# Optimization experiments

Hardware: AMD Instinct MI355X
Metric: run time of the kernel (lower is better)

The kernel has to match this reference:

```python
import jax, jax.numpy as jnp
import numpy as np

B, N, M, H, NH = 128, 4096, 64, 512, 4
IN, OUT = 256, 256
NH2 = 2 * NH  # read/write heads interleaved: even idx = read, odd idx = write
EPS = 1e-8


def setup_inputs() -> dict:
    key = jax.random.key(0)
    ks = jax.random.split(key, 20)
    nrm = lambda k, shape, s=0.05: (jax.random.normal(k, shape, jnp.float32) * s)
    return {
        'in_data': jax.random.normal(ks[0], (B, IN), jnp.float32),
        'memory': jax.random.normal(ks[1], (B, N, M), jnp.float32) * 0.1,
        'h_prev': jax.random.normal(ks[2], (B, H), jnp.float32),
        'c_prev': jax.random.normal(ks[3], (B, H), jnp.float32),
        'prev_reads': jax.random.normal(ks[4], (NH, B, M), jnp.float32),
        'prev_weights': jax.random.uniform(ks[5], (NH2, B, N), jnp.float32),
        # controller LSTMCell (input = in_data ++ prev_reads)
        'W_ih': nrm(ks[6], (4 * H, IN + NH * M)),
        'b_ih': jnp.zeros((4 * H,), jnp.float32),
        'W_hh': nrm(ks[7], (4 * H, H)),
        'b_hh': jnp.zeros((4 * H,), jnp.float32),
        # output layer over [h ++ reads]
        'W_out': nrm(ks[8], (OUT, H + NH * M)),
        'b_out': jnp.zeros((OUT,), jnp.float32),
        # per-head addressing params, stacked over the 2*NH heads (fed with c-state)
        'Wk': nrm(ks[9], (NH2, M, H)), 'bk': jnp.zeros((NH2, M), jnp.float32),
        'Wbeta': nrm(ks[10], (NH2, H)), 'bbeta': jnp.zeros((NH2,), jnp.float32),
        'Wg': nrm(ks[11], (NH2, H)), 'bg': jnp.zeros((NH2,), jnp.float32),
        'Ws': nrm(ks[12], (NH2, 3, H)), 'bs': jnp.zeros((NH2, 3), jnp.float32),
        'Wgam': nrm(ks[13], (NH2, H)), 'bgam': jnp.zeros((NH2,), jnp.float32),
        'We': nrm(ks[14], (NH2, M, H)), 'be': jnp.zeros((NH2, M), jnp.float32),
        'Wa': nrm(ks[15], (NH2, M, H)), 'ba': jnp.zeros((NH2, M), jnp.float32),
    }


def reference(in_data, memory, h_prev, c_prev, prev_reads, prev_weights,
              W_ih, b_ih, W_hh, b_hh, W_out, b_out,
              Wk, bk, Wbeta, bbeta, Wg, bg, Ws, bs, Wgam, bgam, We, be, Wa, ba):
    bsz = in_data.shape[0]
    # controller LSTM step on [x ++ prev_reads]
    x = jnp.concatenate([in_data, jnp.swapaxes(prev_reads, 0, 1).reshape(bsz, -1)], axis=-1)
    gates = x @ W_ih.T + h_prev @ W_hh.T + b_ih + b_hh
    gi, gf, gg, go = jnp.split(gates, 4, axis=-1)
    c = jax.nn.sigmoid(gf) * c_prev + jax.nn.sigmoid(gi) * jnp.tanh(gg)
    h = jax.nn.sigmoid(go) * jnp.tanh(c)  # |h| < 1, so clamp(-20, 20) is identity

    mem = memory
    reads = []
    for i in range(NH2):  # fixed small loop; even = read head, odd = write head
        keyv = c @ Wk[i].T + bk[i]                                    # [B, M]
        beta = jax.nn.softplus(c @ Wbeta[i] + bbeta[i])[:, None]      # [B, 1]
        g = jax.nn.sigmoid(c @ Wg[i] + bg[i])[:, None]                # [B, 1]
        s = jax.nn.softmax(c @ Ws[i].T + bs[i], axis=-1)              # [B, 3]
        gamma = 1.0 + jax.nn.softplus(c @ Wgam[i] + bgam[i])[:, None]  # [B, 1]
        # content addressing: cosine similarity, sharpened softmax
        sim = jnp.einsum('bnm,bm->bn', mem, keyv)
        sim = sim / (jnp.linalg.norm(mem, axis=-1) * jnp.linalg.norm(keyv, axis=-1, keepdims=True) + EPS)
        wc = jax.nn.softmax(beta * sim, axis=-1)
        # interpolate, circular shift (-1, 0, +1), sharpen
        wg_ = g * wc + (1.0 - g) * prev_weights[i]
        wsft = (s[:, 0:1] * jnp.roll(wg_, -1, axis=1)
                + s[:, 1:2] * wg_
                + s[:, 2:3] * jnp.roll(wg_, 1, axis=1))
        wpow = wsft ** gamma
        w = wpow / (jnp.sum(wpow, axis=1, keepdims=True) + EPS)
        if i % 2 == 0:
            reads.append(jnp.einsum('bn,bnm->bm', w, mem))
        else:
            e = jax.nn.sigmoid(c @ We[i].T + be[i])                   # erase [B, M]
            a = jnp.tanh(c @ Wa[i].T + ba[i])                         # add   [B, M]
            mem = mem * (1.0 - w[:, :, None] * e[:, None, :]) + w[:, :, None] * a[:, None, :]

    out = jax.nn.sigmoid(jnp.concatenate([h] + reads, axis=-1) @ W_out.T + b_out)
    return out
```

## Files before the change

### kernel.cpp

```cpp
#include <hip/hip_runtime.h>
#include <math.h>

#define BSZ 128
#define NN_ 4096
#define MM_ 64
#define HH_ 512
#define EPSF 1e-8f

__device__ __forceinline__ float sigmoidf_(float x) { return 1.0f / (1.0f + expf(-x)); }
__device__ __forceinline__ float softplusf_(float x) { return fmaxf(x, 0.0f) + log1pf(expf(-fabsf(x))); }

__global__ void k_build_x(const float* __restrict__ in_data, const float* __restrict__ prev_reads,
                          float* __restrict__ x) {
    int idx = blockIdx.x * blockDim.x + threadIdx.x;
    if (idx >= BSZ * 512) return;
    int b = idx >> 9, j = idx & 511;
    float v;
    if (j < 256) v = in_data[b * 256 + j];
    else {
        int hi = (j - 256) >> 6, m = (j - 256) & 63;
        v = prev_reads[(hi * BSZ + b) * 64 + m];
    }
    x[idx] = v;
}

__global__ __launch_bounds__(256) void k_gemm_atk(const float* __restrict__ A,
                                                  const float* __restrict__ W,
                                                  float* __restrict__ C, int Ncols, int K) {
    __shared__ float Alds[64 * 129];
    __shared__ float Wlds[64 * 65];
    int t = threadIdx.x;
    int k0 = blockIdx.y * 64;
    int n0 = blockIdx.x * 64;
    for (int i = 0; i < 8; ++i) {
        int f = t + 256 * i;
        int row = f >> 4, kk = (f & 15) * 4;
        float4 v = *(const float4*)(A + (size_t)row * K + k0 + kk);
        Alds[(kk + 0) * 129 + row] = v.x;
        Alds[(kk + 1) * 129 + row] = v.y;
        Alds[(kk + 2) * 129 + row] = v.z;
        Alds[(kk + 3) * 129 + row] = v.w;
    }
    for (int i = 0; i < 4; ++i) {
        int f = t + 256 * i;
        int o = f >> 4, kk = (f & 15) * 4;
        float4 v = *(const float4*)(W + (size_t)(n0 + o) * K + k0 + kk);
        Wlds[(kk + 0) * 65 + o] = v.x;
        Wlds[(kk + 1) * 65 + o] = v.y;
        Wlds[(kk + 2) * 65 + o] = v.z;
        Wlds[(kk + 3) * 65 + o] = v.w;
    }
    __syncthreads();
    int ob = (t & 15) * 4;
    int bb = (t >> 4) * 8;
    float acc[4][8];
#pragma unroll
    for (int i = 0; i < 4; ++i)
#pragma unroll
        for (int j = 0; j < 8; ++j) acc[i][j] = 0.f;
    for (int kk = 0; kk < 64; ++kk) {
        const float* wp = &Wlds[kk * 65 + ob];
        const float* ap = &Alds[kk * 129 + bb];
        float w0 = wp[0], w1 = wp[1], w2 = wp[2], w3 = wp[3];
#pragma unroll
        for (int j = 0; j < 8; ++j) {
            float av = ap[j];
            acc[0][j] = fmaf(w0, av, acc[0][j]);
            acc[1][j] = fmaf(w1, av, acc[1][j]);
            acc[2][j] = fmaf(w2, av, acc[2][j]);
            acc[3][j] = fmaf(w3, av, acc[3][j]);
        }
    }
#pragma unroll
    for (int i = 0; i < 4; ++i)
#pragma unroll
        for (int j = 0; j < 8; ++j)
            atomicAdd(&C[(size_t)(bb + j) * Ncols + n0 + ob + i], acc[i][j]);
}

__global__ void k_lstm(const float* __restrict__ gates, const float* __restrict__ b_ih,
                       const float* __restrict__ b_hh, const float* __restrict__ c_prev,
                       float* __restrict__ cbuf, float* __restrict__ hbuf) {
    int idx = blockIdx.x * blockDim.x + threadIdx.x;
    if (idx >= BSZ * HH_) return;
    int b = idx >> 9, j = idx & 511;
    const float* gr = gates + (size_t)b * 2048;
    float gi = gr[j]        + b_ih[j]        + b_hh[j];
    float gf = gr[512 + j]  + b_ih[512 + j]  + b_hh[512 + j];
    float gg = gr[1024 + j] + b_ih[1024 + j] + b_hh[1024 + j];
    float go = gr[1536 + j] + b_ih[1536 + j] + b_hh[1536 + j];
    float cc = sigmoidf_(gf) * c_prev[idx] + sigmoidf_(gi) * tanhf(gg);
    float hh = sigmoidf_(go) * tanhf(cc);
    cbuf[idx] = cc;
    hbuf[idx] = hh;
}

__global__ void k_build_whead(const float* __restrict__ Wk, const float* __restrict__ bk,
                              const float* __restrict__ Wbeta, const float* __restrict__ bbeta,
                              const float* __restrict__ Wg, const float* __restrict__ bg,
                              const float* __restrict__ Ws, const float* __restrict__ bs,
                              const float* __restrict__ Wgam, const float* __restrict__ bgam,
                              const float* __restrict__ We, const float* __restrict__ be,
                              const float* __restrict__ Wa, const float* __restrict__ ba,
                              float* __restrict__ Whead, float* __restrict__ bhead) {
    int idx = blockIdx.x * blockDim.x + threadIdx.x;
    if (idx >= 1600 * 512) return;
    int r = idx >> 9, k = idx & 511;
    float v = 0.f, bv = 0.f;
    if (r < 1584) {
        int i = r / 198, q = r - i * 198;
        if (q < 64)       { v = Wk[((i << 6) + q) * 512 + k];        bv = bk[(i << 6) + q]; }
        else if (q == 64) { v = Wbeta[i * 512 + k];                  bv = bbeta[i]; }
        else if (q == 65) { v = Wg[i * 512 + k];                     bv = bg[i]; }
        else if (q <= 68) { v = Ws[(i * 3 + q - 66) * 512 + k];      bv = bs[i * 3 + q - 66]; }
        else if (q == 69) { v = Wgam[i * 512 + k];                   bv = bgam[i]; }
        else if (q < 134) { v = We[((i << 6) + q - 70) * 512 + k];   bv = be[(i << 6) + q - 70]; }
        else              { v = Wa[((i << 6) + q - 134) * 512 + k];  bv = ba[(i << 6) + q - 134]; }
    }
    Whead[idx] = v;
    if (k == 0) bhead[r] = bv;
}

__global__ __launch_bounds__(256) void k_headact(const float* __restrict__ Chead, const float* __restrict__ bhead,
                                                 float* __restrict__ keys, float* __restrict__ knorm,
                                                 float* __restrict__ betaA, float* __restrict__ gA,
                                                 float* __restrict__ gammaA, float* __restrict__ sA,
                                                 float* __restrict__ eA, float* __restrict__ aA) {
    __shared__ float sk[64];
    __shared__ float s3[3];
    int blk = blockIdx.x;
    int i = blk >> 7, b = blk & 127;
    int q = threadIdx.x;
    float val = 0.f;
    if (q < 198) val = Chead[(size_t)b * 1600 + i * 198 + q] + bhead[i * 198 + q];
    if (q < 64) { keys[(size_t)(i * BSZ + b) * 64 + q] = val; sk[q] = val * val; }
    if (q >= 66 && q <= 68) s3[q - 66] = val;
    __syncthreads();
    if (q == 0) {
        float s = 0.f;
        for (int m2 = 0; m2 < 64; ++m2) s += sk[m2];
        knorm[i * BSZ + b] = sqrtf(s);
    }
    if (q == 64) betaA[i * BSZ + b] = softplusf_(val);
    if (q == 65) gA[i * BSZ + b] = sigmoidf_(val);
    if (q == 69) gammaA[i * BSZ + b] = 1.f + softplusf_(val);
    if (q == 66) {
        float mx = fmaxf(s3[0], fmaxf(s3[1], s3[2]));
        float e0 = expf(s3[0] - mx), e1 = expf(s3[1] - mx), e2 = expf(s3[2] - mx);
        float inv = 1.f / (e0 + e1 + e2);
        sA[(i * BSZ + b) * 3 + 0] = e0 * inv;
        sA[(i * BSZ + b) * 3 + 1] = e1 * inv;
        sA[(i * BSZ + b) * 3 + 2] = e2 * inv;
    }
    if (q >= 70 && q < 134)  eA[(size_t)(i * BSZ + b) * 64 + (q - 70)] = sigmoidf_(val);
    if (q >= 134 && q < 198) aA[(size_t)(i * BSZ + b) * 64 + (q - 134)] = tanhf(val);
}

__global__ __launch_bounds__(256) void k_pass2(const float* __restrict__ mem,
                                               const float* __restrict__ wbuf,
                                               const float* __restrict__ eA, const float* __restrict__ aA,
                                               const float* __restrict__ keys, const float* __restrict__ knorm,
                                               float* __restrict__ sims, float* __restrict__ r_out,
                                               int napply, int nsims, int sh0, int sh1,
                                               int read_state, int read_head, int read_idx) {
    __shared__ __align__(16) float rbuf[16][64];
    int t = threadIdx.x;
    int lane = t & 15, grp = t >> 4;
    int base = blockIdx.x * 64;
    int b = base >> 12;
    int m4 = lane * 4;
    float4 e1 = *(const float4*)(eA + (size_t)(1 * BSZ + b) * 64 + m4);
    float4 a1 = *(const float4*)(aA + (size_t)(1 * BSZ + b) * 64 + m4);
    float4 e3 = *(const float4*)(eA + (size_t)(3 * BSZ + b) * 64 + m4);
    float4 a3 = *(const float4*)(aA + (size_t)(3 * BSZ + b) * 64 + m4);
    float4 e5 = *(const float4*)(eA + (size_t)(5 * BSZ + b) * 64 + m4);
    float4 a5 = *(const float4*)(aA + (size_t)(5 * BSZ + b) * 64 + m4);
    float4 k0v = make_float4(0.f, 0.f, 0.f, 0.f), k1v = k0v;
    float kn0v = 0.f, kn1v = 0.f;
    if (nsims > 0) { k0v = *(const float4*)(keys + (size_t)(sh0 * BSZ + b) * 64 + m4); kn0v = knorm[sh0 * BSZ + b]; }
    if (nsims > 1) { k1v = *(const float4*)(keys + (size_t)(sh1 * BSZ + b) * 64 + m4); kn1v = knorm[sh1 * BSZ + b]; }
    const float* w1p = wbuf + (size_t)1 * BSZ * NN_;
    const float* w3p = wbuf + (size_t)3 * BSZ * NN_;
    const float* w5p = wbuf + (size_t)5 * BSZ * NN_;
    const float* wrp = (read_head >= 0) ? (wbuf + (size_t)read_head * BSZ * NN_) : nullptr;
    float* sim0 = sims + (size_t)sh0 * BSZ * NN_;
    float* sim1 = sims + (size_t)sh1 * BSZ * NN_;

    float4 racc = make_float4(0.f, 0.f, 0.f, 0.f);
    for (int it = 0; it < 4; ++it) {
        int row = base + it * 16 + grp;
        float4 m = *(const float4*)(mem + (size_t)row * 64 + m4);
        float4 mr = m;
        if (napply >= 1) {
            float w = w1p[row];
            m.x = m.x * (1.f - w * e1.x) + w * a1.x;
            m.y = m.y * (1.f - w * e1.y) + w * a1.y;
            m.z = m.z * (1.f - w * e1.z) + w * a1.z;
            m.w = m.w * (1.f - w * e1.w) + w * a1.w;
            if (read_state == 1) mr = m;
        }
        if (napply >= 2) {
            float w = w3p[row];
            m.x = m.x * (1.f - w * e3.x) + w * a3.x;
            m.y = m.y * (1.f - w * e3.y) + w * a3.y;
            m.z = m.z * (1.f - w * e3.z) + w * a3.z;
            m.w = m.w * (1.f - w * e3.w) + w * a3.w;
            if (read_state == 2) mr = m;
        }
        if (napply >= 3) {
            float w = w5p[row];
            m.x = m.x * (1.f - w * e5.x) + w * a5.x;
            m.y = m.y * (1.f - w * e5.y) + w * a5.y;
            m.z = m.z * (1.f - w * e5.z) + w * a5.z;
            m.w = m.w * (1.f - w * e5.w) + w * a5.w;
            if (read_state == 3) mr = m;
        }
        if (read_head >= 0) {
            float wr = wrp[row];
            racc.x = fmaf(wr, mr.x, racc.x);
            racc.y = fmaf(wr, mr.y, racc.y);
            racc.z = fmaf(wr, mr.z, racc.z);
            racc.w = fmaf(wr, mr.w, racc.w);
        }
        if (nsims > 0) {
            float d0 = m.x * k0v.x + m.y * k0v.y + m.z * k0v.z + m.w * k0v.w;
            float nn = m.x * m.x + m.y * m.y + m.z * m.z + m.w * m.w;
            float d1 = 0.f;
            if (nsims > 1) d1 = m.x * k1v.x + m.y * k1v.y + m.z * k1v.z + m.w * k1v.w;
#pragma unroll
            for (int off = 8; off >= 1; off >>= 1) {
                d0 += __shfl_xor(d0, off, 16);
                nn += __shfl_xor(nn, off, 16);
                if (nsims > 1) d1 += __shfl_xor(d1, off, 16);
            }
            if (lane == 0) {
                float nm = sqrtf(nn);
                sim0[row] = d0 / (nm * kn0v + EPSF);
                if (nsims > 1) sim1[row] = d1 / (nm * kn1v + EPSF);
            }
        }
    }
    if (read_head >= 0) {
        *(float4*)(&rbuf[grp][m4]) = racc;
        __syncthreads();
        if (t < 64) {
            float s = 0.f;
#pragma unroll
            for (int g2 = 0; g2 < 16; ++g2) s += rbuf[g2][t];
            atomicAdd(&r_out[(size_t)(read_idx * BSZ + b) * 64 + t], s);
        }
    }
}

__global__ __launch_bounds__(256) void k_weights(const float* __restrict__ sims,
                                                 const float* __restrict__ prev_w,
                                                 const float* __restrict__ betaA, const float* __restrict__ gA,
                                                 const float* __restrict__ gammaA, const float* __restrict__ sA,
                                                 float* __restrict__ wout_base, int head0) {
    __shared__ float wg[NN_];
    __shared__ float red[256];
    int h = head0 + blockIdx.y, b = blockIdx.x;
    int hb = h * BSZ + b;
    float beta = betaA[hb], g = gA[hb], gamma = gammaA[hb];
    float s0 = sA[hb * 3 + 0], s1 = sA[hb * 3 + 1], s2 = sA[hb * 3 + 2];
    const float* sim = sims + (size_t)hb * NN_;
    const float* pw = prev_w + (size_t)hb * NN_;
    float* wout = wout_base + (size_t)hb * NN_;
    int t = threadIdx.x;
    float tv[16];
    float lmax = -3.4e38f;
#pragma unroll
    for (int j = 0; j < 16; ++j) {
        float x = beta * sim[t + 256 * j];
        tv[j] = x;
        lmax = fmaxf(lmax, x);
    }
    red[t] = lmax; __syncthreads();
    for (int s = 128; s > 0; s >>= 1) { if (t < s) red[t] = fmaxf(red[t], red[t + s]); __syncthreads(); }
    float Mx = red[0]; __syncthreads();
    float lsum = 0.f;
#pragma unroll
    for (int j = 0; j < 16; ++j) { float ex = expf(tv[j] - Mx); tv[j] = ex; lsum += ex; }
    red[t] = lsum; __syncthreads();
    for (int s = 128; s > 0; s >>= 1) { if (t < s) red[t] += red[t + s]; __syncthreads(); }
    float invS = 1.f / red[0]; __syncthreads();
#pragma unroll
    for (int j = 0; j < 16; ++j) {
        int n = t + 256 * j;
        wg[n] = g * tv[j] * invS + (1.f - g) * pw[n];
    }
    __syncthreads();
    float lsum2 = 0.f;
#pragma unroll
    for (int j = 0; j < 16; ++j) {
        int n = t + 256 * j;
        float wsft = s0 * wg[(n + 1) & (NN_ - 1)] + s1 * wg[n] + s2 * wg[(n - 1) & (NN_ - 1)];
        float wp = powf(wsft, gamma);
        tv[j] = wp;
        lsum2 += wp;
    }
    red[t] = lsum2; __syncthreads();
    for (int s = 128; s > 0; s >>= 1) { if (t < s) red[t] += red[t + s]; __syncthreads(); }
    float inv2 = 1.f / (red[0] + EPSF);
#pragma unroll
    for (int j = 0; j < 16; ++j) wout[t + 256 * j] = tv[j] * inv2;
}

__global__ void k_build_cat(const float* __restrict__ hbuf, const float* __restrict__ rbuf,
                            float* __restrict__ cat) {
    int idx = blockIdx.x * blockDim.x + threadIdx.x;
    if (idx >= BSZ * 768) return;
    int b = idx / 768, j = idx - b * 768;
    float v;
    if (j < 512) v = hbuf[b * 512 + j];
    else {
        int ri = (j - 512) >> 6, m = (j - 512) & 63;
        v = rbuf[(ri * BSZ + b) * 64 + m];
    }
    cat[idx] = v;
}

__global__ void k_out(const float* __restrict__ outacc, const float* __restrict__ b_out,
                      float* __restrict__ out) {
    int idx = blockIdx.x * blockDim.x + threadIdx.x;
    if (idx >= BSZ * 256) return;
    out[idx] = sigmoidf_(outacc[idx] + b_out[idx & 255]);
}

extern "C" void kernel_launch(void* const* d_in, const int* in_sizes, int n_in,
                              void* d_out, int out_size, void* d_ws, size_t ws_size,
                              hipStream_t stream) {
    const float* in_data      = (const float*)d_in[0];
    const float* memory       = (const float*)d_in[1];
    const float* h_prev       = (const float*)d_in[2];
    const float* c_prev       = (const float*)d_in[3];
    const float* prev_reads   = (const float*)d_in[4];
    const float* prev_weights = (const float*)d_in[5];
    const float* W_ih = (const float*)d_in[6];
    const float* b_ih = (const float*)d_in[7];
    const float* W_hh = (const float*)d_in[8];
    const float* b_hh = (const float*)d_in[9];
    const float* W_out = (const float*)d_in[10];
    const float* b_out = (const float*)d_in[11];
    const float* Wk   = (const float*)d_in[12];
    const float* bk   = (const float*)d_in[13];
    const float* Wbeta = (const float*)d_in[14];
    const float* bbeta = (const float*)d_in[15];
    const float* Wg   = (const float*)d_in[16];
    const float* bg   = (const float*)d_in[17];
    const float* Ws   = (const float*)d_in[18];
    const float* bs   = (const float*)d_in[19];
    const float* Wgam = (const float*)d_in[20];
    const float* bgam = (const float*)d_in[21];
    const float* We   = (const float*)d_in[22];
    const float* be   = (const float*)d_in[23];
    const float* Wa   = (const float*)d_in[24];
    const float* ba   = (const float*)d_in[25];

    float* ws = (float*)d_ws;
    size_t o_gates  = 0;
    size_t o_chead  = o_gates + 262144;
    size_t o_r      = o_chead + 204800;
    size_t o_outacc = o_r + 32768;
    size_t zero_floats = o_outacc + 32768;
    size_t o_x     = zero_floats;
    size_t o_c     = o_x + 65536;
    size_t o_h     = o_c + 65536;
    size_t o_whead = o_h + 65536;
    size_t o_bhead = o_whead + 819200;
    size_t o_keys  = o_bhead + 2048;
    size_t o_knorm = o_keys + 65536;
    size_t o_beta  = o_knorm + 1024;
    size_t o_g     = o_beta + 1024;
    size_t o_gamma = o_g + 1024;
    size_t o_s     = o_gamma + 1024;
    size_t o_e     = o_s + 3072;
    size_t o_a     = o_e + 65536;
    size_t o_sims  = o_a + 65536;
    size_t o_w     = o_sims + 4194304;
    size_t o_cat   = o_w + 4194304;

    float* gates  = ws + o_gates;
    float* Chead  = ws + o_chead;
    float* rbuf   = ws + o_r;
    float* outacc = ws + o_outacc;
    float* xbuf   = ws + o_x;
    float* cbuf   = ws + o_c;
    float* hbuf   = ws + o_h;
    float* Whead  = ws + o_whead;
    float* bhead  = ws + o_bhead;
    float* keys   = ws + o_keys;
    float* knorm  = ws + o_knorm;
    float* betaA  = ws + o_beta;
    float* gA     = ws + o_g;
    float* gammaA = ws + o_gamma;
    float* sA     = ws + o_s;
    float* eA     = ws + o_e;
    float* aA     = ws + o_a;
    float* sims   = ws + o_sims;
    float* wbuf   = ws + o_w;
    float* cat    = ws + o_cat;

    hipMemsetAsync(d_ws, 0, zero_floats * sizeof(float), stream);

    k_build_x<<<256, 256, 0, stream>>>(in_data, prev_reads, xbuf);
    k_gemm_atk<<<dim3(32, 8), 256, 0, stream>>>(xbuf, W_ih, gates, 2048, 512);
    k_gemm_atk<<<dim3(32, 8), 256, 0, stream>>>(h_prev, W_hh, gates, 2048, 512);
    k_lstm<<<256, 256, 0, stream>>>(gates, b_ih, b_hh, c_prev, cbuf, hbuf);

    k_build_whead<<<3200, 256, 0, stream>>>(Wk, bk, Wbeta, bbeta, Wg, bg, Ws, bs,
                                            Wgam, bgam, We, be, Wa, ba, Whead, bhead);
    k_gemm_atk<<<dim3(25, 8), 256, 0, stream>>>(cbuf, Whead, Chead, 1600, 512);
    k_headact<<<1024, 256, 0, stream>>>(Chead, bhead, keys, knorm, betaA, gA, gammaA, sA, eA, aA);

    const int PB = BSZ * NN_ / 64;
    k_pass2<<<PB, 256, 0, stream>>>(memory, wbuf, eA, aA, keys, knorm, sims, rbuf,
                                    0, 2, 0, 1, -1, -1, 0);
    k_weights<<<dim3(128, 2), 256, 0, stream>>>(sims, prev_weights, betaA, gA, gammaA, sA, wbuf, 0);
    k_pass2<<<PB, 256, 0, stream>>>(memory, wbuf, eA, aA, keys, knorm, sims, rbuf,
                                    1, 2, 2, 3, 0, 0, 0);
    k_weights<<<dim3(128, 2), 256, 0, stream>>>(sims, prev_weights, betaA, gA, gammaA, sA, wbuf, 2);
    k_pass2<<<PB, 256, 0, stream>>>(memory, wbuf, eA, aA, keys, knorm, sims, rbuf,
                                    2, 2, 4, 5, 1, 2, 1);
    k_weights<<<dim3(128, 2), 256, 0, stream>>>(sims, prev_weights, betaA, gA, gammaA, sA, wbuf, 4);
    k_pass2<<<PB, 256, 0, stream>>>(memory, wbuf, eA, aA, keys, knorm, sims, rbuf,
                                    3, 1, 6, 6, 2, 4, 2);
    k_weights<<<dim3(128, 1), 256, 0, stream>>>(sims, prev_weights, betaA, gA, gammaA, sA, wbuf, 6);
    k_pass2<<<PB, 256, 0, stream>>>(memory, wbuf, eA, aA, keys, knorm, sims, rbuf,
                                    3, 0, 0, 0, 3, 6, 3);

    k_build_cat<<<384, 256, 0, stream>>>(hbuf, rbuf, cat);
    k_gemm_atk<<<dim3(4, 12), 256, 0, stream>>>(cat, W_out, outacc, 256, 768);
    k_out<<<128, 256, 0, stream>>>(outacc, b_out, (float*)d_out);

    (void)in_sizes; (void)n_in; (void)out_size; (void)ws_size;
}
```

Before: 556.3 us.

## Fuse gather kernels into GEMM loads and widen weights kernel to 1024 threads

Removes the x-build, Whead-build and concat kernels by gathering inputs and head weight rows directly inside specialised GEMM tile loads. The two gate GEMMs become one launch with K=1024, the head GEMM trims padding from 1600 to 1408 columns, and head biases are read straight from the original arrays. The weights kernel moves to 1024 threads per block and uses wave shuffle reductions instead of a shared-memory tree. This is meant to cut launches and intermediate buffer traffic. The cost is more branchy address computation in the GEMM load loops.

```diff
diff --git a/kernel.cpp b/kernel.cpp
--- a/kernel.cpp
+++ b/kernel.cpp
@@ -10,23 +10,12 @@
 __device__ __forceinline__ float sigmoidf_(float x) { return 1.0f / (1.0f + expf(-x)); }
 __device__ __forceinline__ float softplusf_(float x) { return fmaxf(x, 0.0f) + log1pf(expf(-fabsf(x))); }
 
-__global__ void k_build_x(const float* __restrict__ in_data, const float* __restrict__ prev_reads,
-                          float* __restrict__ x) {
-    int idx = blockIdx.x * blockDim.x + threadIdx.x;
-    if (idx >= BSZ * 512) return;
-    int b = idx >> 9, j = idx & 511;
-    float v;
-    if (j < 256) v = in_data[b * 256 + j];
-    else {
-        int hi = (j - 256) >> 6, m = (j - 256) & 63;
-        v = prev_reads[(hi * BSZ + b) * 64 + m];
-    }
-    x[idx] = v;
-}
-
-__global__ __launch_bounds__(256) void k_gemm_atk(const float* __restrict__ A,
-                                                  const float* __restrict__ W,
-                                                  float* __restrict__ C, int Ncols, int K) {
+__global__ __launch_bounds__(256) void k_gemm_gates(const float* __restrict__ in_data,
+                                                    const float* __restrict__ prev_reads,
+                                                    const float* __restrict__ h_prev,
+                                                    const float* __restrict__ W_ih,
+                                                    const float* __restrict__ W_hh,
+                                                    float* __restrict__ C) {
     __shared__ float Alds[64 * 129];
     __shared__ float Wlds[64 * 65];
     int t = threadIdx.x;
@@ -35,7 +24,13 @@
     for (int i = 0; i < 8; ++i) {
         int f = t + 256 * i;
         int row = f >> 4, kk = (f & 15) * 4;
-        float4 v = *(const float4*)(A + (size_t)row * K + k0 + kk);
+        int k = k0 + kk;
+        float4 v;
+        if (k < 256) v = *(const float4*)(in_data + (row << 8) + k);
+        else if (k < 512) {
+            int q = k - 256;
+            v = *(const float4*)(prev_reads + (((q >> 6) * BSZ + row) << 6) + (q & 63));
+        } else v = *(const float4*)(h_prev + (row << 9) + (k - 512));
         Alds[(kk + 0) * 129 + row] = v.x;
         Alds[(kk + 1) * 129 + row] = v.y;
         Alds[(kk + 2) * 129 + row] = v.z;
@@ -44,7 +39,10 @@
     for (int i = 0; i < 4; ++i) {
         int f = t + 256 * i;
         int o = f >> 4, kk = (f & 15) * 4;
-        float4 v = *(const float4*)(W + (size_t)(n0 + o) * K + k0 + kk);
+        int j = n0 + o, k = k0 + kk;
+        const float* src = (k < 512) ? (W_ih + (size_t)j * 512 + k)
+                                     : (W_hh + (size_t)j * 512 + (k - 512));
+        float4 v = *(const float4*)src;
         Wlds[(kk + 0) * 65 + o] = v.x;
         Wlds[(kk + 1) * 65 + o] = v.y;
         Wlds[(kk + 2) * 65 + o] = v.z;
@@ -75,7 +73,147 @@
     for (int i = 0; i < 4; ++i)
 #pragma unroll
         for (int j = 0; j < 8; ++j)
-            atomicAdd(&C[(size_t)(bb + j) * Ncols + n0 + ob + i], acc[i][j]);
+            atomicAdd(&C[(size_t)(bb + j) * 2048 + n0 + ob + i], acc[i][j]);
+}
+
+__device__ __forceinline__ const float* whead_row_ptr(const float* Wk, const float* Wbeta,
+                                                      const float* Wg, const float* Ws,
+                                                      const float* Wgam, const float* We,
+                                                      const float* Wa, int r) {
+    int i = r / 198, q = r - i * 198;
+    if (q < 64)  return Wk + (size_t)((i << 6) + q) * 512;
+    if (q == 64) return Wbeta + (size_t)i * 512;
+    if (q == 65) return Wg + (size_t)i * 512;
+    if (q <= 68) return Ws + (size_t)(i * 3 + q - 66) * 512;
+    if (q == 69) return Wgam + (size_t)i * 512;
+    if (q < 134) return We + (size_t)((i << 6) + q - 70) * 512;
+    return Wa + (size_t)((i << 6) + q - 134) * 512;
+}
+
+__global__ __launch_bounds__(256) void k_gemm_head(const float* __restrict__ A,
+                                                   const float* __restrict__ Wk,
+                                                   const float* __restrict__ Wbeta,
+                                                   const float* __restrict__ Wg,
+                                                   const float* __restrict__ Ws,
+                                                   const float* __restrict__ Wgam,
+                                                   const float* __restrict__ We,
+                                                   const float* __restrict__ Wa,
+                                                   float* __restrict__ C) {
+    __shared__ float Alds[64 * 129];
+    __shared__ float Wlds[64 * 65];
+    int t = threadIdx.x;
+    int k0 = blockIdx.y * 64;
+    int n0 = blockIdx.x * 64;
+    for (int i = 0; i < 8; ++i) {
+        int f = t + 256 * i;
+        int row = f >> 4, kk = (f & 15) * 4;
+        float4 v = *(const float4*)(A + (size_t)row * 512 + k0 + kk);
+        Alds[(kk + 0) * 129 + row] = v.x;
+        Alds[(kk + 1) * 129 + row] = v.y;
+        Alds[(kk + 2) * 129 + row] = v.z;
+        Alds[(kk + 3) * 129 + row] = v.w;
+    }
+    for (int i = 0; i < 4; ++i) {
+        int f = t + 256 * i;
+        int o = f >> 4, kk = (f & 15) * 4;
+        int r = n0 + o;
+        float4 v = make_float4(0.f, 0.f, 0.f, 0.f);
+        if (r < 1386) {
+            const float* p = whead_row_ptr(Wk, Wbeta, Wg, Ws, Wgam, We, Wa, r) + k0 + kk;
+            v = *(const float4*)p;
+        }
+        Wlds[(kk + 0) * 65 + o] = v.x;
+        Wlds[(kk + 1) * 65 + o] = v.y;
+        Wlds[(kk + 2) * 65 + o] = v.z;
+        Wlds[(kk + 3) * 65 + o] = v.w;
+    }
+    __syncthreads();
+    int ob = (t & 15) * 4;
+    int bb = (t >> 4) * 8;
+    float acc[4][8];
+#pragma unroll
+    for (int i = 0; i < 4; ++i)
+#pragma unroll
+        for (int j = 0; j < 8; ++j) acc[i][j] = 0.f;
+    for (int kk = 0; kk < 64; ++kk) {
+        const float* wp = &Wlds[kk * 65 + ob];
+        const float* ap = &Alds[kk * 129 + bb];
+        float w0 = wp[0], w1 = wp[1], w2 = wp[2], w3 = wp[3];
+#pragma unroll
+        for (int j = 0; j < 8; ++j) {
+            float av = ap[j];
+            acc[0][j] = fmaf(w0, av, acc[0][j]);
+            acc[1][j] = fmaf(w1, av, acc[1][j]);
+            acc[2][j] = fmaf(w2, av, acc[2][j]);
+            acc[3][j] = fmaf(w3, av, acc[3][j]);
+        }
+    }
+#pragma unroll
+    for (int i = 0; i < 4; ++i)
+#pragma unroll
+        for (int j = 0; j < 8; ++j)
+            atomicAdd(&C[(size_t)(bb + j) * 1408 + n0 + ob + i], acc[i][j]);
+}
+
+__global__ __launch_bounds__(256) void k_gemm_out(const float* __restrict__ hbuf,
+                                                  const float* __restrict__ rbuf,
+                                                  const float* __restrict__ W_out,
+                                                  float* __restrict__ C) {
+    __shared__ float Alds[64 * 129];
+    __shared__ float Wlds[64 * 65];
+    int t = threadIdx.x;
+    int k0 = blockIdx.y * 64;
+    int n0 = blockIdx.x * 64;
+    for (int i = 0; i < 8; ++i) {
+        int f = t + 256 * i;
+        int row = f >> 4, kk = (f & 15) * 4;
+        int k = k0 + kk;
+        float4 v;
+        if (k < 512) v = *(const float4*)(hbuf + (row << 9) + k);
+        else {
+            int q = k - 512;
+            v = *(const float4*)(rbuf + (((q >> 6) * BSZ + row) << 6) + (q & 63));
+        }
+        Alds[(kk + 0) * 129 + row] = v.x;
+        Alds[(kk + 1) * 129 + row] = v.y;
+        Alds[(kk + 2) * 129 + row] = v.z;
+        Alds[(kk + 3) * 129 + row] = v.w;
+    }
+    for (int i = 0; i < 4; ++i) {
+        int f = t + 256 * i;
+        int o = f >> 4, kk = (f & 15) * 4;
+        float4 v = *(const float4*)(W_out + (size_t)(n0 + o) * 768 + k0 + kk);
+        Wlds[(kk + 0) * 65 + o] = v.x;
+        Wlds[(kk + 1) * 65 + o] = v.y;
+        Wlds[(kk + 2) * 65 + o] = v.z;
+        Wlds[(kk + 3) * 65 + o] = v.w;
+    }
+    __syncthreads();
+    int ob = (t & 15) * 4;
+    int bb = (t >> 4) * 8;
+    float acc[4][8];
+#pragma unroll
+    for (int i = 0; i < 4; ++i)
+#pragma unroll
+        for (int j = 0; j < 8; ++j) acc[i][j] = 0.f;
+    for (int kk = 0; kk < 64; ++kk) {
+        const float* wp = &Wlds[kk * 65 + ob];
+        const float* ap = &Alds[kk * 129 + bb];
+        float w0 = wp[0], w1 = wp[1], w2 = wp[2], w3 = wp[3];
+#pragma unroll
+        for (int j = 0; j < 8; ++j) {
+            float av = ap[j];
+            acc[0][j] = fmaf(w0, av, acc[0][j]);
+            acc[1][j] = fmaf(w1, av, acc[1][j]);
+            acc[2][j] = fmaf(w2, av, acc[2][j]);
+            acc[3][j] = fmaf(w3, av, acc[3][j]);
+        }
+    }
+#pragma unroll
+    for (int i = 0; i < 4; ++i)
+#pragma unroll
+        for (int j = 0; j < 8; ++j)
+            atomicAdd(&C[(size_t)(bb + j) * 256 + n0 + ob + i], acc[i][j]);
 }
 
 __global__ void k_lstm(const float* __restrict__ gates, const float* __restrict__ b_ih,
@@ -95,33 +233,11 @@
     hbuf[idx] = hh;
 }
 
-__global__ void k_build_whead(const float* __restrict__ Wk, const float* __restrict__ bk,
-                              const float* __restrict__ Wbeta, const float* __restrict__ bbeta,
-                              const float* __restrict__ Wg, const float* __restrict__ bg,
-                              const float* __restrict__ Ws, const float* __restrict__ bs,
-                              const float* __restrict__ Wgam, const float* __restrict__ bgam,
-                              const float* __restrict__ We, const float* __restrict__ be,
-                              const float* __restrict__ Wa, const float* __restrict__ ba,
-                              float* __restrict__ Whead, float* __restrict__ bhead) {
-    int idx = blockIdx.x * blockDim.x + threadIdx.x;
-    if (idx >= 1600 * 512) return;
-    int r = idx >> 9, k = idx & 511;
-    float v = 0.f, bv = 0.f;
-    if (r < 1584) {
-        int i = r / 198, q = r - i * 198;
-        if (q < 64)       { v = Wk[((i << 6) + q) * 512 + k];        bv = bk[(i << 6) + q]; }
-        else if (q == 64) { v = Wbeta[i * 512 + k];                  bv = bbeta[i]; }
-        else if (q == 65) { v = Wg[i * 512 + k];                     bv = bg[i]; }
-        else if (q <= 68) { v = Ws[(i * 3 + q - 66) * 512 + k];      bv = bs[i * 3 + q - 66]; }
-        else if (q == 69) { v = Wgam[i * 512 + k];                   bv = bgam[i]; }
-        else if (q < 134) { v = We[((i << 6) + q - 70) * 512 + k];   bv = be[(i << 6) + q - 70]; }
-        else              { v = Wa[((i << 6) + q - 134) * 512 + k];  bv = ba[(i << 6) + q - 134]; }
-    }
-    Whead[idx] = v;
-    if (k == 0) bhead[r] = bv;
-}
-
-__global__ __launch_bounds__(256) void k_headact(const float* __restrict__ Chead, const float* __restrict__ bhead,
+__global__ __launch_bounds__(256) void k_headact(const float* __restrict__ Chead,
+                                                 const float* __restrict__ bk, const float* __restrict__ bbeta,
+                                                 const float* __restrict__ bg, const float* __restrict__ bs,
+                                                 const float* __restrict__ bgam, const float* __restrict__ be,
+                                                 const float* __restrict__ ba,
                                                  float* __restrict__ keys, float* __restrict__ knorm,
                                                  float* __restrict__ betaA, float* __restrict__ gA,
                                                  float* __restrict__ gammaA, float* __restrict__ sA,
@@ -132,7 +248,16 @@
     int i = blk >> 7, b = blk & 127;
     int q = threadIdx.x;
     float val = 0.f;
-    if (q < 198) val = Chead[(size_t)b * 1600 + i * 198 + q] + bhead[i * 198 + q];
+    if (q < 198) {
+        float bv = (q < 64)   ? bk[(i << 6) + q]
+                 : (q == 64)  ? bbeta[i]
+                 : (q == 65)  ? bg[i]
+                 : (q <= 68)  ? bs[i * 3 + q - 66]
+                 : (q == 69)  ? bgam[i]
+                 : (q < 134)  ? be[(i << 6) + q - 70]
+                              : ba[(i << 6) + q - 134];
+        val = Chead[(size_t)b * 1408 + i * 198 + q] + bv;
+    }
     if (q < 64) { keys[(size_t)(i * BSZ + b) * 64 + q] = val; sk[q] = val * val; }
     if (q >= 66 && q <= 68) s3[q - 66] = val;
     __syncthreads();
@@ -252,13 +377,13 @@
     }
 }
 
-__global__ __launch_bounds__(256) void k_weights(const float* __restrict__ sims,
-                                                 const float* __restrict__ prev_w,
-                                                 const float* __restrict__ betaA, const float* __restrict__ gA,
-                                                 const float* __restrict__ gammaA, const float* __restrict__ sA,
-                                                 float* __restrict__ wout_base, int head0) {
+__global__ __launch_bounds__(1024) void k_weights(const float* __restrict__ sims,
+                                                  const float* __restrict__ prev_w,
+                                                  const float* __restrict__ betaA, const float* __restrict__ gA,
+                                                  const float* __restrict__ gammaA, const float* __restrict__ sA,
+                                                  float* __restrict__ wout_base, int head0) {
     __shared__ float wg[NN_];
-    __shared__ float red[256];
+    __shared__ float redm[16], reds[16], redp[16];
     int h = head0 + blockIdx.y, b = blockIdx.x;
     int hb = h * BSZ + b;
     float beta = betaA[hb], g = gA[hb], gamma = gammaA[hb];
@@ -266,58 +391,58 @@
     const float* sim = sims + (size_t)hb * NN_;
     const float* pw = prev_w + (size_t)hb * NN_;
     float* wout = wout_base + (size_t)hb * NN_;
-    int t = threadIdx.x;
-    float tv[16];
+    int t = threadIdx.x, wv = t >> 6, ln = t & 63;
+    float tv[4];
     float lmax = -3.4e38f;
 #pragma unroll
-    for (int j = 0; j < 16; ++j) {
-        float x = beta * sim[t + 256 * j];
+    for (int j = 0; j < 4; ++j) {
+        float x = beta * sim[t + 1024 * j];
         tv[j] = x;
         lmax = fmaxf(lmax, x);
     }
-    red[t] = lmax; __syncthreads();
-    for (int s = 128; s > 0; s >>= 1) { if (t < s) red[t] = fmaxf(red[t], red[t + s]); __syncthreads(); }
-    float Mx = red[0]; __syncthreads();
+#pragma unroll
+    for (int off = 32; off >= 1; off >>= 1) lmax = fmaxf(lmax, __shfl_xor(lmax, off));
+    if (ln == 0) redm[wv] = lmax;
+    __syncthreads();
+    float Mx = redm[0];
+#pragma unroll
+    for (int k = 1; k < 16; ++k) Mx = fmaxf(Mx, redm[k]);
     float lsum = 0.f;
 #pragma unroll
-    for (int j = 0; j < 16; ++j) { float ex = expf(tv[j] - Mx); tv[j] = ex; lsum += ex; }
-    red[t] = lsum; __syncthreads();
-    for (int s = 128; s > 0; s >>= 1) { if (t < s) red[t] += red[t + s]; __syncthreads(); }
-    float invS = 1.f / red[0]; __syncthreads();
-#pragma unroll
-    for (int j = 0; j < 16; ++j) {
-        int n = t + 256 * j;
+    for (int j = 0; j < 4; ++j) { float ex = expf(tv[j] - Mx); tv[j] = ex; lsum += ex; }
+#pragma unroll
+    for (int off = 32; off >= 1; off >>= 1) lsum += __shfl_xor(lsum, off);
+    if (ln == 0) reds[wv] = lsum;
+    __syncthreads();
+    float S = 0.f;
+#pragma unroll
+    for (int k = 0; k < 16; ++k) S += reds[k];
+    float invS = 1.f / S;
+#pragma unroll
+    for (int j = 0; j < 4; ++j) {
+        int n = t + 1024 * j;
         wg[n] = g * tv[j] * invS + (1.f - g) * pw[n];
     }
     __syncthreads();
     float lsum2 = 0.f;
 #pragma unroll
-    for (int j = 0; j < 16; ++j) {
-        int n = t + 256 * j;
+    for (int j = 0; j < 4; ++j) {
+        int n = t + 1024 * j;
         float wsft = s0 * wg[(n + 1) & (NN_ - 1)] + s1 * wg[n] + s2 * wg[(n - 1) & (NN_ - 1)];
         float wp = powf(wsft, gamma);
         tv[j] = wp;
         lsum2 += wp;
     }
-    red[t] = lsum2; __syncthreads();
-    for (int s = 128; s > 0; s >>= 1) { if (t < s) red[t] += red[t + s]; __syncthreads(); }
-    float inv2 = 1.f / (red[0] + EPSF);
-#pragma unroll
-    for (int j = 0; j < 16; ++j) wout[t + 256 * j] = tv[j] * inv2;
-}
-
-__global__ void k_build_cat(const float* __restrict__ hbuf, const float* __restrict__ rbuf,
-                            float* __restrict__ cat) {
-    int idx = blockIdx.x * blockDim.x + threadIdx.x;
-    if (idx >= BSZ * 768) return;
-    int b = idx / 768, j = idx - b * 768;
-    float v;
-    if (j < 512) v = hbuf[b * 512 + j];
-    else {
-        int ri = (j - 512) >> 6, m = (j - 512) & 63;
-        v = rbuf[(ri * BSZ + b) * 64 + m];
-    }
-    cat[idx] = v;
+#pragma unroll
+    for (int off = 32; off >= 1; off >>= 1) lsum2 += __shfl_xor(lsum2, off);
+    if (ln == 0) redp[wv] = lsum2;
+    __syncthreads();
+    float S2 = 0.f;
+#pragma unroll
+    for (int k = 0; k < 16; ++k) S2 += redp[k];
+    float inv2 = 1.f / (S2 + EPSF);
+#pragma unroll
+    for (int j = 0; j < 4; ++j) wout[t + 1024 * j] = tv[j] * inv2;
 }
 
 __global__ void k_out(const float* __restrict__ outacc, const float* __restrict__ b_out,
@@ -360,35 +485,28 @@
     float* ws = (float*)d_ws;
     size_t o_gates  = 0;
     size_t o_chead  = o_gates + 262144;
-    size_t o_r      = o_chead + 204800;
+    size_t o_r      = o_chead + 180224;
     size_t o_outacc = o_r + 32768;
     size_t zero_floats = o_outacc + 32768;
-    size_t o_x     = zero_floats;
-    size_t o_c     = o_x + 65536;
+    size_t o_c     = zero_floats;
     size_t o_h     = o_c + 65536;
-    size_t o_whead = o_h + 65536;
-    size_t o_bhead = o_whead + 819200;
-    size_t o_keys  = o_bhead + 2048;
-    size_t o_knorm = o_keys + 65536;
+    size_t o_keys  = o_h + 65536;
+    size_t o_knorm = o_keys + 57344;
     size_t o_beta  = o_knorm + 1024;
     size_t o_g     = o_beta + 1024;
     size_t o_gamma = o_g + 1024;
     size_t o_s     = o_gamma + 1024;
     size_t o_e     = o_s + 3072;
-    size_t o_a     = o_e + 65536;
-    size_t o_sims  = o_a + 65536;
-    size_t o_w     = o_sims + 4194304;
-    size_t o_cat   = o_w + 4194304;
+    size_t o_a     = o_e + 57344;
+    size_t o_sims  = o_a + 57344;
+    size_t o_w     = o_sims + 3670016;
 
     float* gates  = ws + o_gates;
     float* Chead  = ws + o_chead;
     float* rbuf   = ws + o_r;
     float* outacc = ws + o_outacc;
-    float* xbuf   = ws + o_x;
     float* cbuf   = ws + o_c;
     float* hbuf   = ws + o_h;
-    float* Whead  = ws + o_whead;
-    float* bhead  = ws + o_bhead;
     float* keys   = ws + o_keys;
     float* knorm  = ws + o_knorm;
     float* betaA  = ws + o_beta;
@@ -399,38 +517,33 @@
     float* aA     = ws + o_a;
     float* sims   = ws + o_sims;
     float* wbuf   = ws + o_w;
-    float* cat    = ws + o_cat;
 
     hipMemsetAsync(d_ws, 0, zero_floats * sizeof(float), stream);
 
-    k_build_x<<<256, 256, 0, stream>>>(in_data, prev_reads, xbuf);
-    k_gemm_atk<<<dim3(32, 8), 256, 0, stream>>>(xbuf, W_ih, gates, 2048, 512);
-    k_gemm_atk<<<dim3(32, 8), 256, 0, stream>>>(h_prev, W_hh, gates, 2048, 512);
+    k_gemm_gates<<<dim3(32, 16), 256, 0, stream>>>(in_data, prev_reads, h_prev, W_ih, W_hh, gates);
     k_lstm<<<256, 256, 0, stream>>>(gates, b_ih, b_hh, c_prev, cbuf, hbuf);
 
-    k_build_whead<<<3200, 256, 0, stream>>>(Wk, bk, Wbeta, bbeta, Wg, bg, Ws, bs,
-                                            Wgam, bgam, We, be, Wa, ba, Whead, bhead);
-    k_gemm_atk<<<dim3(25, 8), 256, 0, stream>>>(cbuf, Whead, Chead, 1600, 512);
-    k_headact<<<1024, 256, 0, stream>>>(Chead, bhead, keys, knorm, betaA, gA, gammaA, sA, eA, aA);
+    k_gemm_head<<<dim3(22, 8), 256, 0, stream>>>(cbuf, Wk, Wbeta, Wg, Ws, Wgam, We, Wa, Chead);
+    k_headact<<<896, 256, 0, stream>>>(Chead, bk, bbeta, bg, bs, bgam, be, ba,
+                                       keys, knorm, betaA, gA, gammaA, sA, eA, aA);
 
     const int PB = BSZ * NN_ / 64;
     k_pass2<<<PB, 256, 0, stream>>>(memory, wbuf, eA, aA, keys, knorm, sims, rbuf,
                                     0, 2, 0, 1, -1, -1, 0);
-    k_weights<<<dim3(128, 2), 256, 0, stream>>>(sims, prev_weights, betaA, gA, gammaA, sA, wbuf, 0);
+    k_weights<<<dim3(128, 2), 1024, 0, stream>>>(sims, prev_weights, betaA, gA, gammaA, sA, wbuf, 0);
     k_pass2<<<PB, 256, 0, stream>>>(memory, wbuf, eA, aA, keys, knorm, sims, rbuf,
                                     1, 2, 2, 3, 0, 0, 0);
-    k_weights<<<dim3(128, 2), 256, 0, stream>>>(sims, prev_weights, betaA, gA, gammaA, sA, wbuf, 2);
+    k_weights<<<dim3(128, 2), 1024, 0, stream>>>(sims, prev_weights, betaA, gA, gammaA, sA, wbuf, 2);
     k_pass2<<<PB, 256, 0, stream>>>(memory, wbuf, eA, aA, keys, knorm, sims, rbuf,
                                     2, 2, 4, 5, 1, 2, 1);
-    k_weights<<<dim3(128, 2), 256, 0, stream>>>(sims, prev_weights, betaA, gA, gammaA, sA, wbuf, 4);
+    k_weights<<<dim3(128, 2), 1024, 0, stream>>>(sims, prev_weights, betaA, gA, gammaA, sA, wbuf, 4);
     k_pass2<<<PB, 256, 0, stream>>>(memory, wbuf, eA, aA, keys, knorm, sims, rbuf,
                                     3, 1, 6, 6, 2, 4, 2);
-    k_weights<<<dim3(128, 1), 256, 0, stream>>>(sims, prev_weights, betaA, gA, gammaA, sA, wbuf, 6);
+    k_weights<<<dim3(128, 1), 1024, 0, stream>>>(sims, prev_weights, betaA, gA, gammaA, sA, wbuf, 6);
     k_pass2<<<PB, 256, 0, stream>>>(memory, wbuf, eA, aA, keys, knorm, sims, rbuf,
                                     3, 0, 0, 0, 3, 6, 3);
 
-    k_build_cat<<<384, 256, 0, stream>>>(hbuf, rbuf, cat);
-    k_gemm_atk<<<dim3(4, 12), 256, 0, stream>>>(cat, W_out, outacc, 256, 768);
+    k_gemm_out<<<dim3(4, 12), 256, 0, stream>>>(hbuf, rbuf, W_out, outacc);
     k_out<<<128, 256, 0, stream>>>(outacc, b_out, (float*)d_out);
 
     (void)in_sizes; (void)n_in; (void)out_size; (void)ws_size;
```

Result: faster. 534.7 us (-3.9%).
